# Kernel tuning notes

Hardware: AMD Instinct MI355X
Metric: run time of the kernel (lower is better)

Reference implementation:

```python
import jax, jax.numpy as jnp
import numpy as np

FEAT = 64
NSPIX = 256

def setup_inputs() -> dict:
    key = jax.random.key(0)
    ks = jax.random.split(key, 10)
    B, H, W = 8, 512, 512
    x = jax.random.normal(ks[0], (B, 3, H, W), dtype=jnp.float32)
    labels = jax.random.randint(ks[1], (B, 1, H, W), 0, NSPIX, dtype=jnp.int32)
    # learned params (1x1 convs as dense matrices, eval-mode BatchNorm stats)
    W_pix = jax.random.normal(ks[2], (FEAT, 3), dtype=jnp.float32) * 0.1
    b_pix = jax.random.normal(ks[3], (FEAT,), dtype=jnp.float32) * 0.01
    W_red = jax.random.normal(ks[4], (FEAT, 2 * FEAT), dtype=jnp.float32) * 0.05
    b_red = jax.random.normal(ks[5], (FEAT,), dtype=jnp.float32) * 0.01
    w_sim = jax.random.normal(ks[6], (1,), dtype=jnp.float32)
    b_sim = jax.random.normal(ks[7], (1,), dtype=jnp.float32) * 0.01
    bn_gamma = jnp.ones((1,), dtype=jnp.float32)
    bn_beta = jnp.zeros((1,), dtype=jnp.float32)
    bn_mean = jnp.zeros((1,), dtype=jnp.float32)
    bn_var = jnp.ones((1,), dtype=jnp.float32)
    return {"x": x, "labels": labels, "num_spixels": NSPIX,
            "W_pix": W_pix, "b_pix": b_pix, "W_red": W_red, "b_red": b_red,
            "w_sim": w_sim, "b_sim": b_sim,
            "bn_gamma": bn_gamma, "bn_beta": bn_beta,
            "bn_mean": bn_mean, "bn_var": bn_var}


def reference(x, labels, num_spixels, W_pix, b_pix, W_red, b_red,
              w_sim, b_sim, bn_gamma, bn_beta, bn_mean, bn_var):
    B, C, H, W = x.shape
    Fdim = W_pix.shape[0]
    # pixel_conv: 1x1 conv == per-pixel dense
    feats = jnp.einsum('fc,bchw->bfhw', W_pix, x) + b_pix[None, :, None, None]
    feats = feats.reshape(B, Fdim, H * W)              # [B, F, HW]
    lab = labels.reshape(B, H * W).astype(jnp.int32)   # [B, HW]
    # fused per-batch segment reduce: offset labels so one segment_sum handles all B
    seg = (lab + jnp.arange(B, dtype=jnp.int32)[:, None] * num_spixels).reshape(-1)
    nseg = B * num_spixels
    feat_flat = feats.transpose(0, 2, 1).reshape(-1, Fdim)       # [B*HW, F]
    count = jax.ops.segment_sum(jnp.ones((B * H * W,), dtype=feats.dtype), seg,
                                num_segments=nseg)
    count = jnp.maximum(count, 1.0).reshape(B, num_spixels, 1)    # [B, S, 1]
    ssum = jax.ops.segment_sum(feat_flat, seg, num_segments=nseg).reshape(B, num_spixels, Fdim)
    ssq = jax.ops.segment_sum(feat_flat * feat_flat, seg, num_segments=nseg).reshape(B, num_spixels, Fdim)
    mean = ssum / count                                           # [B, S, F]
    var = ssq / count - mean * mean
    std = jnp.sqrt(jnp.maximum(var, 1e-6))
    combined = jnp.concatenate([mean, std], axis=-1)              # [B, S, 2F]
    # reduce_conv: 1x1 conv over channel dim
    reduced = jnp.einsum('fg,bsg->bsf', W_red, combined) + b_red  # [B, S, F]
    # F.normalize(p=2, dim=channel) with eps=1e-12
    nrm = jnp.maximum(jnp.sqrt(jnp.sum(reduced * reduced, axis=-1, keepdims=True)), 1e-12)
    rn = reduced / nrm
    sim = jnp.einsum('bsf,btf->bst', rn, rn)                      # [B, S, S]
    # similarity_weight_block: Conv2d(1,1,1) -> BatchNorm2d(1, eval) -> ReLU
    y = sim * w_sim[0] + b_sim[0]
    y = bn_gamma[0] * (y - bn_mean[0]) / jnp.sqrt(bn_var[0] + 1e-5) + bn_beta[0]
    y = jax.nn.relu(y)
    return y[:, None, :, :]                                       # [B, 1, S, S]
```

## Files before the change

### kernel.cpp

```cpp
#include <hip/hip_runtime.h>

#define HW   262144
#define HW4  65536
#define NSEG 256
#define NB   8

__global__ __launch_bounds__(256) void k_moments(const float* __restrict__ x,
                                                 const int* __restrict__ labels,
                                                 float* __restrict__ part) {
  __shared__ unsigned cnt[NSEG];
  __shared__ unsigned offs[NSEG];
  __shared__ unsigned wtot[4];
  __shared__ __align__(16) float buf[2048][4];
  const int t = threadIdx.x, w = t >> 6, lane = t & 63;
  const int b = blockIdx.x >> 7, blk = blockIdx.x & 127;

  cnt[t] = 0u;
  __syncthreads();

  const float4* __restrict__ x4 = (const float4*)(x + (size_t)b * 3 * HW);
  const int4*  __restrict__ l4  = (const int4*)(labels + (size_t)b * HW);

  float4 A0[2], A1[2], A2[2];
  int lb[8];
  unsigned rk[8];

  #pragma unroll
  for (int it = 0; it < 2; ++it) {
    const int g = blk * 512 + w * 128 + it * 64 + lane;
    A0[it] = x4[g];
    A1[it] = x4[HW4 + g];
    A2[it] = x4[2 * HW4 + g];
    int4 lv = l4[g];
    lb[it * 4 + 0] = lv.x; lb[it * 4 + 1] = lv.y;
    lb[it * 4 + 2] = lv.z; lb[it * 4 + 3] = lv.w;
  }

  #pragma unroll
  for (int k = 0; k < 8; ++k) rk[k] = atomicAdd(&cnt[lb[k]], 1u);
  __syncthreads();

  const unsigned v = cnt[t];
  unsigned inc = v;
  #pragma unroll
  for (int off = 1; off < 64; off <<= 1) {
    unsigned u = __shfl_up(inc, off, 64);
    if (lane >= off) inc += u;
  }
  if (lane == 63) wtot[w] = inc;
  __syncthreads();
  unsigned wbase = 0;
  #pragma unroll
  for (int i = 0; i < 3; ++i) if (i < w) wbase += wtot[i];
  offs[t] = wbase + inc - v;
  __syncthreads();

  #pragma unroll
  for (int it = 0; it < 2; ++it) {
    float c0[4] = {A0[it].x, A0[it].y, A0[it].z, A0[it].w};
    float c1[4] = {A1[it].x, A1[it].y, A1[it].z, A1[it].w};
    float c2[4] = {A2[it].x, A2[it].y, A2[it].z, A2[it].w};
    #pragma unroll
    for (int k = 0; k < 4; ++k) {
      const int p = it * 4 + k;
      const unsigned pos = offs[lb[p]] + rk[p];
      *(float4*)&buf[pos][0] = make_float4(c0[k], c1[k], c2[k], 0.f);
    }
  }
  __syncthreads();

  const unsigned n = cnt[t], base = offs[t];
  float s0 = 0.f, s1 = 0.f, s2 = 0.f;
  float q00 = 0.f, q11 = 0.f, q22 = 0.f, q01 = 0.f, q02 = 0.f, q12 = 0.f;
  for (unsigned i = 0; i < n; ++i) {
    float4 p = *(const float4*)&buf[base + i][0];
    s0 += p.x;  s1 += p.y;  s2 += p.z;
    q00 += p.x * p.x;  q11 += p.y * p.y;  q22 += p.z * p.z;
    q01 += p.x * p.y;  q02 += p.x * p.z;  q12 += p.y * p.z;
  }

  float* o = part + (size_t)blockIdx.x * 2560;
  o[0 * NSEG + t] = (float)n;
  o[1 * NSEG + t] = s0;   o[2 * NSEG + t] = s1;   o[3 * NSEG + t] = s2;
  o[4 * NSEG + t] = q00;  o[5 * NSEG + t] = q11;  o[6 * NSEG + t] = q22;
  o[7 * NSEG + t] = q01;  o[8 * NSEG + t] = q02;  o[9 * NSEG + t] = q12;
}

__global__ __launch_bounds__(256) void k_reduce(const float* __restrict__ part,
                                                float* __restrict__ acc) {
  const int b = blockIdx.x / 10, m = blockIdx.x % 10;
  const float* p = part + (size_t)(b * 128) * 2560 + m * 256 + threadIdx.x;
  float s0 = 0.f, s1 = 0.f, s2 = 0.f, s3 = 0.f;
  for (int i = 0; i < 128; i += 4) {
    s0 += p[(size_t)(i + 0) * 2560];
    s1 += p[(size_t)(i + 1) * 2560];
    s2 += p[(size_t)(i + 2) * 2560];
    s3 += p[(size_t)(i + 3) * 2560];
  }
  acc[(size_t)(b * 10 + m) * 256 + threadIdx.x] = (s0 + s1) + (s2 + s3);
}

__global__ __launch_bounds__(256) void k_stats(const float* __restrict__ acc,
                                               const float* __restrict__ W_pix,
                                               const float* __restrict__ b_pix,
                                               const float* __restrict__ W_red,
                                               const float* __restrict__ b_red,
                                               float* __restrict__ rn) {
  __shared__ float wred[64 * 129];
  __shared__ float comb[4][132];
  const int t = threadIdx.x;

  for (int j4 = t; j4 < 2048; j4 += 256) {
    const int row = j4 >> 5;
    const int c4  = (j4 & 31) << 2;
    float4 v = ((const float4*)W_red)[j4];
    float* d = &wred[row * 129 + c4];
    d[0] = v.x; d[1] = v.y; d[2] = v.z; d[3] = v.w;
  }
  __syncthreads();

  const int w = t >> 6;
  const int f = t & 63;
  const int seg = blockIdx.x * 4 + w;
  const int b = seg >> 8;
  const int s = seg & 255;

  const float* a = acc + b * (10 * NSEG);
  const float N   = fmaxf(a[0 * NSEG + s], 1.0f);
  const float S0  = a[1 * NSEG + s];
  const float S1  = a[2 * NSEG + s];
  const float S2  = a[3 * NSEG + s];
  const float M00 = a[4 * NSEG + s];
  const float M11 = a[5 * NSEG + s];
  const float M22 = a[6 * NSEG + s];
  const float M01 = a[7 * NSEG + s];
  const float M02 = a[8 * NSEG + s];
  const float M12 = a[9 * NSEG + s];

  const float w0 = W_pix[f * 3 + 0];
  const float w1 = W_pix[f * 3 + 1];
  const float w2 = W_pix[f * 3 + 2];
  const float bf = b_pix[f];

  const float wS   = w0 * S0 + w1 * S1 + w2 * S2;
  const float mean = (wS + N * bf) / N;
  const float ssq  = w0 * w0 * M00 + w1 * w1 * M11 + w2 * w2 * M22
                   + 2.f * (w0 * w1 * M01 + w0 * w2 * M02 + w1 * w2 * M12)
                   + 2.f * bf * wS + N * bf * bf;
  const float var  = ssq / N - mean * mean;
  const float stdv = sqrtf(fmaxf(var, 1e-6f));

  comb[w][f]      = mean;
  comb[w][64 + f] = stdv;
  __syncthreads();

  float r = b_red[f];
  const float* wr = &wred[f * 129];
  const float* cb = comb[w];
  for (int g = 0; g < 128; ++g) r += wr[g] * cb[g];

  float sq = r * r;
  #pragma unroll
  for (int off = 32; off > 0; off >>= 1) sq += __shfl_xor(sq, off, 64);
  const float inv = 1.0f / fmaxf(sqrtf(sq), 1e-12f);

  rn[(size_t)seg * 64 + f] = r * inv;
}

__global__ __launch_bounds__(256) void k_sim(const float* __restrict__ rn,
                                             float* __restrict__ out,
                                             const float* __restrict__ w_sim,
                                             const float* __restrict__ b_sim,
                                             const float* __restrict__ bn_g,
                                             const float* __restrict__ bn_b,
                                             const float* __restrict__ bn_m,
                                             const float* __restrict__ bn_v) {
  __shared__ float A[64 * 65];
  __shared__ float Bt[64 * 65];
  const int t  = threadIdx.x;
  const int b  = blockIdx.x >> 4;
  const int ti = (blockIdx.x >> 2) & 3;
  const int tj = blockIdx.x & 3;

  const float4* rn4 = (const float4*)(rn + (size_t)b * NSEG * 64);
  for (int j4 = t; j4 < 1024; j4 += 256) {
    const int row = j4 >> 4;
    const int c4  = (j4 & 15) << 2;
    float4 va = rn4[(ti * 64 + row) * 16 + (j4 & 15)];
    float* da = &A[row * 65 + c4];
    da[0] = va.x; da[1] = va.y; da[2] = va.z; da[3] = va.w;
    float4 vb = rn4[(tj * 64 + row) * 16 + (j4 & 15)];
    float* db = &Bt[row * 65 + c4];
    db[0] = vb.x; db[1] = vb.y; db[2] = vb.z; db[3] = vb.w;
  }
  __syncthreads();

  const int tx = t & 15;
  const int ty = t >> 4;
  float acc[4][4] = {{0.f}};
  for (int k = 0; k < 64; ++k) {
    float av[4], bv[4];
    #pragma unroll
    for (int i = 0; i < 4; ++i) av[i] = A[(ty * 4 + i) * 65 + k];
    #pragma unroll
    for (int j = 0; j < 4; ++j) bv[j] = Bt[(tx * 4 + j) * 65 + k];
    #pragma unroll
    for (int i = 0; i < 4; ++i)
      #pragma unroll
      for (int j = 0; j < 4; ++j) acc[i][j] += av[i] * bv[j];
  }

  const float invsd = 1.0f / sqrtf(bn_v[0] + 1e-5f);
  const float scale = w_sim[0] * bn_g[0] * invsd;
  const float shift = (b_sim[0] - bn_m[0]) * bn_g[0] * invsd + bn_b[0];

  #pragma unroll
  for (int i = 0; i < 4; ++i) {
    float4 v;
    v.x = fmaxf(acc[i][0] * scale + shift, 0.f);
    v.y = fmaxf(acc[i][1] * scale + shift, 0.f);
    v.z = fmaxf(acc[i][2] * scale + shift, 0.f);
    v.w = fmaxf(acc[i][3] * scale + shift, 0.f);
    const int base = b * 65536 + (ti * 64 + ty * 4 + i) * 256 + tj * 64;
    ((float4*)out)[(base >> 2) + tx] = v;
  }
}

extern "C" void kernel_launch(void* const* d_in, const int* in_sizes, int n_in,
                              void* d_out, int out_size, void* d_ws, size_t ws_size,
                              hipStream_t stream) {
  (void)in_sizes; (void)n_in; (void)out_size; (void)ws_size;
  const float* x      = (const float*)d_in[0];
  const int*   labels = (const int*)d_in[1];
  const float* W_pix  = (const float*)d_in[3];
  const float* b_pix  = (const float*)d_in[4];
  const float* W_red  = (const float*)d_in[5];
  const float* b_red  = (const float*)d_in[6];
  const float* w_sim  = (const float*)d_in[7];
  const float* b_sim  = (const float*)d_in[8];
  const float* bn_g   = (const float*)d_in[9];
  const float* bn_b   = (const float*)d_in[10];
  const float* bn_m   = (const float*)d_in[11];
  const float* bn_v   = (const float*)d_in[12];
  float* out = (float*)d_out;

  float* part = (float*)d_ws;
  float* acc  = part + (size_t)1024 * 2560;
  float* rn   = acc + NB * 10 * NSEG;

  k_moments<<<dim3(1024), dim3(256), 0, stream>>>(x, labels, part);
  k_reduce<<<dim3(80), dim3(256), 0, stream>>>(part, acc);
  k_stats<<<dim3(512), dim3(256), 0, stream>>>(acc, W_pix, b_pix, W_red, b_red, rn);
  k_sim<<<dim3(128), dim3(256), 0, stream>>>(rn, out, w_sim, b_sim, bn_g, bn_b, bn_m, bn_v);
}
```

Baseline: 117.0 us.

## Halve pixels per moments block and split the partial reduction into four chunks

k_moments now launches 2048 blocks, each handling 1024 pixels instead of 2048, which halves the LDS sort buffer and should allow more resident blocks. k_reduce is split into four chunks per batch/moment (320 blocks), and k_stats sums the four chunk partials. The aim is more parallelism and occupancy in the first two stages. The cost is twice as much partial-sum traffic and more per-segment scan overhead relative to useful work.

```diff
diff --git a/kernel.cpp b/kernel.cpp
--- a/kernel.cpp
+++ b/kernel.cpp
@@ -11,9 +11,9 @@
   __shared__ unsigned cnt[NSEG];
   __shared__ unsigned offs[NSEG];
   __shared__ unsigned wtot[4];
-  __shared__ __align__(16) float buf[2048][4];
+  __shared__ __align__(16) float buf[1024][4];
   const int t = threadIdx.x, w = t >> 6, lane = t & 63;
-  const int b = blockIdx.x >> 7, blk = blockIdx.x & 127;
+  const int b = blockIdx.x >> 8, blk = blockIdx.x & 255;
 
   cnt[t] = 0u;
   __syncthreads();
@@ -21,23 +21,16 @@
   const float4* __restrict__ x4 = (const float4*)(x + (size_t)b * 3 * HW);
   const int4*  __restrict__ l4  = (const int4*)(labels + (size_t)b * HW);
 
-  float4 A0[2], A1[2], A2[2];
-  int lb[8];
-  unsigned rk[8];
-
-  #pragma unroll
-  for (int it = 0; it < 2; ++it) {
-    const int g = blk * 512 + w * 128 + it * 64 + lane;
-    A0[it] = x4[g];
-    A1[it] = x4[HW4 + g];
-    A2[it] = x4[2 * HW4 + g];
-    int4 lv = l4[g];
-    lb[it * 4 + 0] = lv.x; lb[it * 4 + 1] = lv.y;
-    lb[it * 4 + 2] = lv.z; lb[it * 4 + 3] = lv.w;
-  }
-
-  #pragma unroll
-  for (int k = 0; k < 8; ++k) rk[k] = atomicAdd(&cnt[lb[k]], 1u);
+  const int g = blk * 256 + t;
+  float4 A0 = x4[g];
+  float4 A1 = x4[HW4 + g];
+  float4 A2 = x4[2 * HW4 + g];
+  int4  lv  = l4[g];
+  int lb[4] = {lv.x, lv.y, lv.z, lv.w};
+  unsigned rk[4];
+
+  #pragma unroll
+  for (int k = 0; k < 4; ++k) rk[k] = atomicAdd(&cnt[lb[k]], 1u);
   __syncthreads();
 
   const unsigned v = cnt[t];
@@ -55,17 +48,13 @@
   offs[t] = wbase + inc - v;
   __syncthreads();
 
-  #pragma unroll
-  for (int it = 0; it < 2; ++it) {
-    float c0[4] = {A0[it].x, A0[it].y, A0[it].z, A0[it].w};
-    float c1[4] = {A1[it].x, A1[it].y, A1[it].z, A1[it].w};
-    float c2[4] = {A2[it].x, A2[it].y, A2[it].z, A2[it].w};
-    #pragma unroll
-    for (int k = 0; k < 4; ++k) {
-      const int p = it * 4 + k;
-      const unsigned pos = offs[lb[p]] + rk[p];
-      *(float4*)&buf[pos][0] = make_float4(c0[k], c1[k], c2[k], 0.f);
-    }
+  float c0[4] = {A0.x, A0.y, A0.z, A0.w};
+  float c1[4] = {A1.x, A1.y, A1.z, A1.w};
+  float c2[4] = {A2.x, A2.y, A2.z, A2.w};
+  #pragma unroll
+  for (int k = 0; k < 4; ++k) {
+    const unsigned pos = offs[lb[k]] + rk[k];
+    *(float4*)&buf[pos][0] = make_float4(c0[k], c1[k], c2[k], 0.f);
   }
   __syncthreads();
 
@@ -88,16 +77,17 @@
 
 __global__ __launch_bounds__(256) void k_reduce(const float* __restrict__ part,
                                                 float* __restrict__ acc) {
-  const int b = blockIdx.x / 10, m = blockIdx.x % 10;
-  const float* p = part + (size_t)(b * 128) * 2560 + m * 256 + threadIdx.x;
+  const int bm = blockIdx.x >> 2, c = blockIdx.x & 3;
+  const int b = bm / 10, m = bm % 10;
+  const float* p = part + ((size_t)(b * 256 + c * 64)) * 2560 + m * 256 + threadIdx.x;
   float s0 = 0.f, s1 = 0.f, s2 = 0.f, s3 = 0.f;
-  for (int i = 0; i < 128; i += 4) {
+  for (int i = 0; i < 64; i += 4) {
     s0 += p[(size_t)(i + 0) * 2560];
     s1 += p[(size_t)(i + 1) * 2560];
     s2 += p[(size_t)(i + 2) * 2560];
     s3 += p[(size_t)(i + 3) * 2560];
   }
-  acc[(size_t)(b * 10 + m) * 256 + threadIdx.x] = (s0 + s1) + (s2 + s3);
+  acc[(size_t)((b * 4 + c) * 10 + m) * 256 + threadIdx.x] = (s0 + s1) + (s2 + s3);
 }
 
 __global__ __launch_bounds__(256) void k_stats(const float* __restrict__ acc,
@@ -125,17 +115,19 @@
   const int b = seg >> 8;
   const int s = seg & 255;
 
-  const float* a = acc + b * (10 * NSEG);
-  const float N   = fmaxf(a[0 * NSEG + s], 1.0f);
-  const float S0  = a[1 * NSEG + s];
-  const float S1  = a[2 * NSEG + s];
-  const float S2  = a[3 * NSEG + s];
-  const float M00 = a[4 * NSEG + s];
-  const float M11 = a[5 * NSEG + s];
-  const float M22 = a[6 * NSEG + s];
-  const float M01 = a[7 * NSEG + s];
-  const float M02 = a[8 * NSEG + s];
-  const float M12 = a[9 * NSEG + s];
+  float mm[10];
+  #pragma unroll
+  for (int m = 0; m < 10; ++m) {
+    float v = 0.f;
+    #pragma unroll
+    for (int c = 0; c < 4; ++c)
+      v += acc[(size_t)((b * 4 + c) * 10 + m) * 256 + s];
+    mm[m] = v;
+  }
+  const float N   = fmaxf(mm[0], 1.0f);
+  const float S0  = mm[1], S1 = mm[2], S2 = mm[3];
+  const float M00 = mm[4], M11 = mm[5], M22 = mm[6];
+  const float M01 = mm[7], M02 = mm[8], M12 = mm[9];
 
   const float w0 = W_pix[f * 3 + 0];
   const float w1 = W_pix[f * 3 + 1];
@@ -245,11 +237,11 @@
   float* out = (float*)d_out;
 
   float* part = (float*)d_ws;
-  float* acc  = part + (size_t)1024 * 2560;
-  float* rn   = acc + NB * 10 * NSEG;
-
-  k_moments<<<dim3(1024), dim3(256), 0, stream>>>(x, labels, part);
-  k_reduce<<<dim3(80), dim3(256), 0, stream>>>(part, acc);
+  float* acc  = part + (size_t)2048 * 2560;
+  float* rn   = acc + NB * 4 * 10 * NSEG;
+
+  k_moments<<<dim3(2048), dim3(256), 0, stream>>>(x, labels, part);
+  k_reduce<<<dim3(320), dim3(256), 0, stream>>>(part, acc);
   k_stats<<<dim3(512), dim3(256), 0, stream>>>(acc, W_pix, b_pix, W_red, b_red, rn);
   k_sim<<<dim3(128), dim3(256), 0, stream>>>(rn, out, w_sim, b_sim, bn_g, bn_b, bn_m, bn_v);
 }
```

Result: no change. 118.6 us (+1.4%).
